# Kernel optimization log

Measured on AMD Instinct MI355X. Metric: run time of the kernel, lower is better.

## Reference

```python
import jax, jax.numpy as jnp
import numpy as np

EPS = 1e-4  # matches init_kwargs eps


def setup_inputs() -> dict:
    key = jax.random.key(0)
    k1, k2, k3 = jax.random.split(key, 3)
    B, C, T = 64, 256, 2048
    x = jax.random.normal(k1, (B, C, T), dtype=jnp.float32)
    # per-timestep BatchNorm affine params: [T, C]
    gamma = 1.0 + 0.1 * jax.random.normal(k2, (T, C), dtype=jnp.float32)
    beta = 0.01 * jax.random.normal(k3, (T, C), dtype=jnp.float32)
    return {"x": x, "gamma": gamma, "beta": beta}


def reference(x, gamma, beta):
    # BNTTv1 (training mode): every timestep's BatchNorm1d sees the FULL [B, C, T]
    # tensor, so the batch statistics (per-channel mean/var over B and T) are
    # identical across timesteps. Only the affine (gamma_t, beta_t) differs, and
    # the module keeps just slice t of layer t's output. Equivalent fused form:
    mean = jnp.mean(x, axis=(0, 2), keepdims=True)            # [1, C, 1]
    var = jnp.mean((x - mean) ** 2, axis=(0, 2), keepdims=True)  # biased var
    norm = (x - mean) * jax.lax.rsqrt(var + EPS)              # [B, C, T]
    # gamma/beta: [T, C] -> broadcast as [1, C, T]
    out = norm * gamma.T[None, :, :] + beta.T[None, :, :]
    return out
```

## Files before the change

### kernel.cpp

```cpp
#include <hip/hip_runtime.h>
#include <hip/hip_bf16.h>

#define B_ 64
#define C_ 256
#define T_ 2048
#define EPS_ 1e-4f
#define NPC ((float)(B_ * T_))

__global__ __launch_bounds__(512) void bntt_init(float* stats) {
    int i = threadIdx.x;
    if (i < 2 * C_) stats[i] = 0.0f;
}

#define SPLITS 8
#define BPB (B_ / SPLITS)

__global__ __launch_bounds__(256) void bntt_stats(const float* __restrict__ x,
                                                  float* __restrict__ stats) {
    const int c  = blockIdx.x & (C_ - 1);
    const int s  = blockIdx.x >> 8;
    const int tid = threadIdx.x;

    float sum = 0.0f, sumsq = 0.0f;
    const int b0 = s * BPB;
    for (int b = b0; b < b0 + BPB; ++b) {
        const float4* p = (const float4*)(x + (size_t)b * (C_ * T_) + (size_t)c * T_);
        #pragma unroll
        for (int i = tid; i < T_ / 4; i += 256) {
            float4 v = p[i];
            sum   += v.x + v.y + v.z + v.w;
            sumsq += v.x * v.x + v.y * v.y + v.z * v.z + v.w * v.w;
        }
    }
    #pragma unroll
    for (int off = 32; off > 0; off >>= 1) {
        sum   += __shfl_down(sum, off);
        sumsq += __shfl_down(sumsq, off);
    }
    __shared__ float ls[4], lss[4];
    const int wave = tid >> 6, lane = tid & 63;
    if (lane == 0) { ls[wave] = sum; lss[wave] = sumsq; }
    __syncthreads();
    if (tid == 0) {
        float S  = ls[0] + ls[1] + ls[2] + ls[3];
        float SS = lss[0] + lss[1] + lss[2] + lss[3];
        atomicAdd(&stats[c], S);
        atomicAdd(&stats[C_ + c], SS);
    }
}

__global__ __launch_bounds__(256) void bntt_finalize(float* stats) {
    int c = threadIdx.x;
    float mean = stats[c] / NPC;
    float var  = stats[C_ + c] / NPC - mean * mean;
    stats[c]       = mean;
    stats[C_ + c]  = rsqrtf(var + EPS_);
}

__global__ __launch_bounds__(1024) void bntt_prep(const float* __restrict__ gamma,
                                                  const float* __restrict__ beta,
                                                  const float* __restrict__ stats,
                                                  float* __restrict__ scale,
                                                  float* __restrict__ shift) {
    __shared__ float tg[32][33];
    __shared__ float tb[32][33];
    const int tx = threadIdx.x & 31;
    const int ty = threadIdx.x >> 5;
    const int c0 = blockIdx.x * 32;
    const int t0 = blockIdx.y * 32;

    tg[ty][tx] = gamma[(size_t)(t0 + ty) * C_ + (c0 + tx)];
    tb[ty][tx] = beta [(size_t)(t0 + ty) * C_ + (c0 + tx)];
    __syncthreads();

    const int c = c0 + ty;
    const float mean = stats[c];
    const float istd = stats[C_ + c];
    const float g = tg[tx][ty];
    const float bb = tb[tx][ty];
    const float sc = g * istd;
    scale[(size_t)c * T_ + (t0 + tx)] = sc;
    shift[(size_t)c * T_ + (t0 + tx)] = fmaf(-mean, sc, bb);
}

__global__ __launch_bounds__(256) void bntt_norm(const float* __restrict__ x,
                                                 const float* __restrict__ scale,
                                                 const float* __restrict__ shift,
                                                 float* __restrict__ out) {
    const int idx4 = blockIdx.x * 256 + threadIdx.x;
    const int t4   = idx4 & (T_ / 4 - 1);
    const int row  = idx4 >> 9;
    const int c    = row & (C_ - 1);

    const float4 xv = ((const float4*)x)[idx4];
    const float4 sc = ((const float4*)(scale + (size_t)c * T_))[t4];
    const float4 sh = ((const float4*)(shift + (size_t)c * T_))[t4];
    float4 o;
    o.x = fmaf(xv.x, sc.x, sh.x);
    o.y = fmaf(xv.y, sc.y, sh.y);
    o.z = fmaf(xv.z, sc.z, sh.z);
    o.w = fmaf(xv.w, sc.w, sh.w);
    ((float4*)out)[idx4] = o;
}

__global__ __launch_bounds__(256) void bntt_norm_fb(const float* __restrict__ x,
                                                    const float* __restrict__ gamma,
                                                    const float* __restrict__ beta,
                                                    const float* __restrict__ stats,
                                                    float* __restrict__ out) {
    const int idx4 = blockIdx.x * 256 + threadIdx.x;
    const int t4   = idx4 & (T_ / 4 - 1);
    const int row  = idx4 >> 9;
    const int c    = row & (C_ - 1);
    const int t    = t4 * 4;

    const float mean = stats[c];
    const float istd = stats[C_ + c];
    const float4 xv = ((const float4*)x)[idx4];
    float4 o;
    #pragma unroll
    for (int j = 0; j < 4; ++j) {
        float g  = gamma[(size_t)(t + j) * C_ + c];
        float bb = beta [(size_t)(t + j) * C_ + c];
        float sc = g * istd;
        float sh = fmaf(-mean, sc, bb);
        float xs = (&xv.x)[j];
        (&o.x)[j] = fmaf(xs, sc, sh);
    }
    ((float4*)out)[idx4] = o;
}

extern "C" void kernel_launch(void* const* d_in, const int* in_sizes, int n_in,
                              void* d_out, int out_size, void* d_ws, size_t ws_size,
                              hipStream_t stream) {
    const float* x     = (const float*)d_in[0];
    const float* gamma = (const float*)d_in[1];
    const float* beta  = (const float*)d_in[2];
    float* out = (float*)d_out;

    float* stats = (float*)d_ws;
    float* scale = stats + 2 * C_;
    float* shift = scale + (size_t)C_ * T_;
    const size_t need = (2 * C_ + 2 * (size_t)C_ * T_) * sizeof(float);

    bntt_init<<<1, 512, 0, stream>>>(stats);
    bntt_stats<<<C_ * SPLITS, 256, 0, stream>>>(x, stats);
    bntt_finalize<<<1, 256, 0, stream>>>(stats);

    const int nvec = B_ * C_ * T_ / 4;
    if (ws_size >= need) {
        dim3 pg(C_ / 32, T_ / 32);
        bntt_prep<<<pg, 1024, 0, stream>>>(gamma, beta, stats, scale, shift);
        bntt_norm<<<nvec / 256, 256, 0, stream>>>(x, scale, shift, out);
    } else {
        bntt_norm_fb<<<nvec / 256, 256, 0, stream>>>(x, gamma, beta, stats, out);
    }
}
```

Measured before the change: 262.0 us.

## Drop atomics and tiny kernels; reuse scale/shift across batch in norm kernel

Replaces the init/atomicAdd/finalize sequence with per-split partial sums written to workspace, which the prep kernel reduces and turns into mean and inverse std itself. This removes two tiny kernel launches and the atomic traffic. The norm kernel now has each thread load scale/shift once and loop over a 32-batch chunk, using nontemporal stores for the output, so parameter loads are cut and the output stream is kept from polluting cache. The trade-off is a smaller grid (1024 blocks) and each prep block redundantly reducing the partials for its channels.

```diff
diff --git a/kernel.cpp b/kernel.cpp
--- a/kernel.cpp
+++ b/kernel.cpp
@@ -7,27 +7,26 @@
 #define EPS_ 1e-4f
 #define NPC ((float)(B_ * T_))
 
-__global__ __launch_bounds__(512) void bntt_init(float* stats) {
-    int i = threadIdx.x;
-    if (i < 2 * C_) stats[i] = 0.0f;
-}
-
 #define SPLITS 8
 #define BPB (B_ / SPLITS)
+#define T4 (T_ / 4)
+
+typedef float f4 __attribute__((ext_vector_type(4)));
 
 __global__ __launch_bounds__(256) void bntt_stats(const float* __restrict__ x,
-                                                  float* __restrict__ stats) {
-    const int c  = blockIdx.x & (C_ - 1);
-    const int s  = blockIdx.x >> 8;
+                                                  float* __restrict__ partials) {
+    const int c   = blockIdx.x & (C_ - 1);
+    const int s   = blockIdx.x >> 8;
     const int tid = threadIdx.x;
 
     float sum = 0.0f, sumsq = 0.0f;
     const int b0 = s * BPB;
-    for (int b = b0; b < b0 + BPB; ++b) {
-        const float4* p = (const float4*)(x + (size_t)b * (C_ * T_) + (size_t)c * T_);
+    #pragma unroll
+    for (int b = 0; b < BPB; ++b) {
+        const f4* p = (const f4*)(x + (size_t)(b0 + b) * (C_ * T_) + (size_t)c * T_);
         #pragma unroll
-        for (int i = tid; i < T_ / 4; i += 256) {
-            float4 v = p[i];
+        for (int i = 0; i < T4 / 256; ++i) {
+            f4 v = p[tid + i * 256];
             sum   += v.x + v.y + v.z + v.w;
             sumsq += v.x * v.x + v.y * v.y + v.z * v.z + v.w * v.w;
         }
@@ -42,92 +41,118 @@
     if (lane == 0) { ls[wave] = sum; lss[wave] = sumsq; }
     __syncthreads();
     if (tid == 0) {
-        float S  = ls[0] + ls[1] + ls[2] + ls[3];
-        float SS = lss[0] + lss[1] + lss[2] + lss[3];
-        atomicAdd(&stats[c], S);
-        atomicAdd(&stats[C_ + c], SS);
+        partials[s * C_ + c]                   = ls[0] + ls[1] + ls[2] + ls[3];
+        partials[SPLITS * C_ + s * C_ + c]     = lss[0] + lss[1] + lss[2] + lss[3];
     }
-}
-
-__global__ __launch_bounds__(256) void bntt_finalize(float* stats) {
-    int c = threadIdx.x;
-    float mean = stats[c] / NPC;
-    float var  = stats[C_ + c] / NPC - mean * mean;
-    stats[c]       = mean;
-    stats[C_ + c]  = rsqrtf(var + EPS_);
 }
 
 __global__ __launch_bounds__(1024) void bntt_prep(const float* __restrict__ gamma,
                                                   const float* __restrict__ beta,
-                                                  const float* __restrict__ stats,
+                                                  const float* __restrict__ partials,
                                                   float* __restrict__ scale,
                                                   float* __restrict__ shift) {
     __shared__ float tg[32][33];
     __shared__ float tb[32][33];
+    __shared__ float smean[32], sistd[32];
     const int tx = threadIdx.x & 31;
     const int ty = threadIdx.x >> 5;
     const int c0 = blockIdx.x * 32;
     const int t0 = blockIdx.y * 32;
 
+    if (threadIdx.x < 32) {
+        const int c = c0 + threadIdx.x;
+        float S = 0.0f, SS = 0.0f;
+        #pragma unroll
+        for (int s = 0; s < SPLITS; ++s) {
+            S  += partials[s * C_ + c];
+            SS += partials[SPLITS * C_ + s * C_ + c];
+        }
+        float mean = S / NPC;
+        float var  = SS / NPC - mean * mean;
+        smean[threadIdx.x] = mean;
+        sistd[threadIdx.x] = rsqrtf(var + EPS_);
+    }
     tg[ty][tx] = gamma[(size_t)(t0 + ty) * C_ + (c0 + tx)];
     tb[ty][tx] = beta [(size_t)(t0 + ty) * C_ + (c0 + tx)];
     __syncthreads();
 
-    const int c = c0 + ty;
-    const float mean = stats[c];
-    const float istd = stats[C_ + c];
-    const float g = tg[tx][ty];
-    const float bb = tb[tx][ty];
-    const float sc = g * istd;
-    scale[(size_t)c * T_ + (t0 + tx)] = sc;
-    shift[(size_t)c * T_ + (t0 + tx)] = fmaf(-mean, sc, bb);
+    const float mean = smean[ty];
+    const float istd = sistd[ty];
+    const float sc = tg[tx][ty] * istd;
+    scale[(size_t)(c0 + ty) * T_ + (t0 + tx)] = sc;
+    shift[(size_t)(c0 + ty) * T_ + (t0 + tx)] = fmaf(-mean, sc, tb[tx][ty]);
 }
 
+#define BCHUNK 32
 __global__ __launch_bounds__(256) void bntt_norm(const float* __restrict__ x,
                                                  const float* __restrict__ scale,
                                                  const float* __restrict__ shift,
                                                  float* __restrict__ out) {
-    const int idx4 = blockIdx.x * 256 + threadIdx.x;
-    const int t4   = idx4 & (T_ / 4 - 1);
-    const int row  = idx4 >> 9;
-    const int c    = row & (C_ - 1);
+    const int p   = (blockIdx.x & 511) * 256 + threadIdx.x;
+    const int c   = p >> 9;
+    const int t4  = p & (T4 - 1);
+    const int b0  = (blockIdx.x >> 9) * BCHUNK;
 
-    const float4 xv = ((const float4*)x)[idx4];
-    const float4 sc = ((const float4*)(scale + (size_t)c * T_))[t4];
-    const float4 sh = ((const float4*)(shift + (size_t)c * T_))[t4];
-    float4 o;
-    o.x = fmaf(xv.x, sc.x, sh.x);
-    o.y = fmaf(xv.y, sc.y, sh.y);
-    o.z = fmaf(xv.z, sc.z, sh.z);
-    o.w = fmaf(xv.w, sc.w, sh.w);
-    ((float4*)out)[idx4] = o;
+    const f4 sc = ((const f4*)scale)[(size_t)c * T4 + t4];
+    const f4 sh = ((const f4*)shift)[(size_t)c * T4 + t4];
+
+    size_t idx = (size_t)(b0 * C_ + c) * T4 + t4;
+    const size_t step = (size_t)C_ * T4;
+    #pragma unroll 4
+    for (int b = 0; b < BCHUNK; ++b) {
+        f4 xv = ((const f4*)x)[idx];
+        f4 o;
+        o.x = fmaf(xv.x, sc.x, sh.x);
+        o.y = fmaf(xv.y, sc.y, sh.y);
+        o.z = fmaf(xv.z, sc.z, sh.z);
+        o.w = fmaf(xv.w, sc.w, sh.w);
+        __builtin_nontemporal_store(o, &((f4*)out)[idx]);
+        idx += step;
+    }
 }
 
 __global__ __launch_bounds__(256) void bntt_norm_fb(const float* __restrict__ x,
                                                     const float* __restrict__ gamma,
                                                     const float* __restrict__ beta,
-                                                    const float* __restrict__ stats,
+                                                    const float* __restrict__ partials,
                                                     float* __restrict__ out) {
-    const int idx4 = blockIdx.x * 256 + threadIdx.x;
-    const int t4   = idx4 & (T_ / 4 - 1);
-    const int row  = idx4 >> 9;
-    const int c    = row & (C_ - 1);
-    const int t    = t4 * 4;
+    const int p   = (blockIdx.x & 511) * 256 + threadIdx.x;
+    const int c   = p >> 9;
+    const int t4  = p & (T4 - 1);
+    const int t   = t4 * 4;
+    const int b0  = (blockIdx.x >> 9) * BCHUNK;
 
-    const float mean = stats[c];
-    const float istd = stats[C_ + c];
-    const float4 xv = ((const float4*)x)[idx4];
-    float4 o;
+    float S = 0.0f, SS = 0.0f;
+    #pragma unroll
+    for (int s = 0; s < SPLITS; ++s) {
+        S  += partials[s * C_ + c];
+        SS += partials[SPLITS * C_ + s * C_ + c];
+    }
+    const float mean = S / NPC;
+    const float istd = rsqrtf(SS / NPC - mean * mean + EPS_);
+
+    f4 sc, sh;
     #pragma unroll
     for (int j = 0; j < 4; ++j) {
         float g  = gamma[(size_t)(t + j) * C_ + c];
         float bb = beta [(size_t)(t + j) * C_ + c];
-        float sc = g * istd;
-        float sh = fmaf(-mean, sc, bb);
-        float xs = (&xv.x)[j];
-        (&o.x)[j] = fmaf(xs, sc, sh);
+        float s1 = g * istd;
+        ((float*)&sc)[j] = s1;
+        ((float*)&sh)[j] = fmaf(-mean, s1, bb);
     }
-    ((float4*)out)[idx4] = o;
+    size_t idx = (size_t)(b0 * C_ + c) * T4 + t4;
+    const size_t step = (size_t)C_ * T4;
+    #pragma unroll 4
+    for (int b = 0; b < BCHUNK; ++b) {
+        f4 xv = ((const f4*)x)[idx];
+        f4 o;
+        o.x = fmaf(xv.x, sc.x, sh.x);
+        o.y = fmaf(xv.y, sc.y, sh.y);
+        o.z = fmaf(xv.z, sc.z, sh.z);
+        o.w = fmaf(xv.w, sc.w, sh.w);
+        __builtin_nontemporal_store(o, &((f4*)out)[idx]);
+        idx += step;
+    }
 }
 
 extern "C" void kernel_launch(void* const* d_in, const int* in_sizes, int n_in,
@@ -138,21 +163,19 @@
     const float* beta  = (const float*)d_in[2];
     float* out = (float*)d_out;
 
-    float* stats = (float*)d_ws;
-    float* scale = stats + 2 * C_;
-    float* shift = scale + (size_t)C_ * T_;
-    const size_t need = (2 * C_ + 2 * (size_t)C_ * T_) * sizeof(float);
+    float* partials = (float*)d_ws;
+    float* scale    = partials + 2 * SPLITS * C_;
+    float* shift    = scale + (size_t)C_ * T_;
+    const size_t need = (2 * SPLITS * C_ + 2 * (size_t)C_ * T_) * sizeof(float);
 
-    bntt_init<<<1, 512, 0, stream>>>(stats);
-    bntt_stats<<<C_ * SPLITS, 256, 0, stream>>>(x, stats);
-    bntt_finalize<<<1, 256, 0, stream>>>(stats);
+    bntt_stats<<<C_ * SPLITS, 256, 0, stream>>>(x, partials);
 
-    const int nvec = B_ * C_ * T_ / 4;
+    const int ngrid = (C_ * T4 / 256) * (B_ / BCHUNK);
     if (ws_size >= need) {
         dim3 pg(C_ / 32, T_ / 32);
-        bntt_prep<<<pg, 1024, 0, stream>>>(gamma, beta, stats, scale, shift);
-        bntt_norm<<<nvec / 256, 256, 0, stream>>>(x, scale, shift, out);
+        bntt_prep<<<pg, 1024, 0, stream>>>(gamma, beta, partials, scale, shift);
+        bntt_norm<<<ngrid, 256, 0, stream>>>(x, scale, shift, out);
     } else {
-        bntt_norm_fb<<<nvec / 256, 256, 0, stream>>>(x, gamma, beta, stats, out);
+        bntt_norm_fb<<<ngrid, 256, 0, stream>>>(x, gamma, beta, partials, out);
     }
 }
```

Measured after the change: 252.3 us. 3.7% less time.
